# Performance work log

Measured on AMD Instinct MI355X. Metric: run time of the kernel, lower is better.

## Reference

```python
import jax, jax.numpy as jnp
import numpy as np

T, B, H, L = 1024, 256, 120, 4  # time, batch, hidden, layers


def setup_inputs() -> dict:
    key = jax.random.key(0)
    ks = jax.random.split(key, 10)
    s = 1.0 / np.sqrt(H)  # PyTorch LSTM init scale
    u = lambda k, shape: jax.random.uniform(k, shape, jnp.float32, -s, s)
    return {
        "x": jax.random.normal(ks[0], (T, B), jnp.float32),
        "h0": jax.random.uniform(ks[1], (L, B, H), jnp.float32),
        "c0": jax.random.uniform(ks[2], (L, B, H), jnp.float32),
        "W_ih0": u(ks[3], (4 * H, 1)),
        "W_ih": u(ks[4], (L - 1, 4 * H, H)),
        "W_hh": u(ks[5], (L, 4 * H, H)),
        "b_ih": u(ks[6], (L, 4 * H)),
        "b_hh": u(ks[7], (L, 4 * H)),
        "W_lin": u(ks[8], (1, H)),
        "b_lin": u(ks[9], (1,)),
    }


def _lstm_cell(x, h, c, gates_x):
    # gates_x: precomputed x @ W_ih^T + b_ih part already folded by caller
    raise NotImplementedError  # unused helper placeholder


def reference(x, h0, c0, W_ih0, W_ih, W_hh, b_ih, b_hh, W_lin, b_lin):
    def step(carry, x_t):
        h, c = carry                      # each [L, B, H]
        inp = x_t[:, None]                # [B, 1]
        new_h, new_c = [], []
        for l in range(L):
            Wih = W_ih0 if l == 0 else W_ih[l - 1]
            gates = inp @ Wih.T + b_ih[l] + h[l] @ W_hh[l].T + b_hh[l]  # [B, 4H]
            i_g, f_g, g_g, o_g = jnp.split(gates, 4, axis=-1)  # PyTorch gate order i,f,g,o
            c_l = jax.nn.sigmoid(f_g) * c[l] + jax.nn.sigmoid(i_g) * jnp.tanh(g_g)
            h_l = jax.nn.sigmoid(o_g) * jnp.tanh(c_l)
            new_h.append(h_l)
            new_c.append(c_l)
            inp = h_l
        out_t = (inp @ W_lin.T + b_lin)[:, 0]  # [B]
        return (jnp.stack(new_h), jnp.stack(new_c)), out_t

    _, outputs = jax.lax.scan(step, (h0, c0), x)  # outputs: [T, B]
    return outputs
```

## Files before the change

### kernel.cpp

```cpp
#include <hip/hip_runtime.h>
#include <hip/hip_fp16.h>
#include <math.h>

#define Tn 1024
#define Bn 256
#define Hn 120
#define Ln 4
#define NBC 16
#define NBCOL 16
#define NBLK (Ln*NBC)
#define THR 512
#define Dd 16
#define PADI 32
#define KPh 392

typedef _Float16 f16x8 __attribute__((ext_vector_type(8)));
typedef float    f32x4 __attribute__((ext_vector_type(4)));
typedef unsigned int u32x4 __attribute__((ext_vector_type(4)));
typedef unsigned short ushort_t;

template<int N> struct IC { static constexpr int value = N; };

__device__ ushort_t g_ring[(size_t)3 * Dd * NBC * NBCOL * Hn];
__device__ int g_prod[3 * NBC * PADI];
__device__ int g_cons[Ln * NBC * PADI];
__device__ int g_abort;

__global__ __launch_bounds__(256) void init_kernel() {
    int idx = threadIdx.x;
    if (idx < 3 * NBC)  g_prod[idx * PADI] = -1;
    if (idx < Ln * NBC) g_cons[idx * PADI] = -1;
    if (idx == 0)       g_abort = 0;
}

#if __has_builtin(__builtin_amdgcn_exp2f)
__device__ __forceinline__ float hw_exp2(float x) { return __builtin_amdgcn_exp2f(x); }
#else
__device__ __forceinline__ float hw_exp2(float x) { return exp2f(x); }
#endif
#if __has_builtin(__builtin_amdgcn_rcpf)
__device__ __forceinline__ float hw_rcp(float x) { return __builtin_amdgcn_rcpf(x); }
#else
__device__ __forceinline__ float hw_rcp(float x) { return 1.0f / x; }
#endif
#define LOG2E_F 1.44269504f

__device__ __forceinline__ float sigm(float v) {
    return hw_rcp(1.0f + hw_exp2(-LOG2E_F * v));
}
__device__ __forceinline__ float tanh_fast(float v) {
    return 1.0f - 2.0f * hw_rcp(1.0f + hw_exp2(2.0f * LOG2E_F * v));
}

#define BAR_LGKM() asm volatile("s_waitcnt lgkmcnt(0)\ns_barrier" ::: "memory")

__device__ __forceinline__ void spin_wait(int* p, int tgt, int& dead, int& pc) {
    if (dead || pc >= tgt) return;
    int guard = 0, v;
    while ((v = __hip_atomic_load(p, __ATOMIC_RELAXED,
                                  __HIP_MEMORY_SCOPE_SYSTEM)) < tgt) {
        __builtin_amdgcn_s_sleep(1);
        if ((++guard & 127) == 0) {
            if (__hip_atomic_load(&g_abort, __ATOMIC_RELAXED,
                                  __HIP_MEMORY_SCOPE_SYSTEM)) { dead = 1; return; }
            if (guard > 60000) { atomicExch(&g_abort, 1); dead = 1; return; }
        }
    }
    pc = v;
}

__device__ __forceinline__ void post_flag(int* p, int v) {
    __hip_atomic_store(p, v, __ATOMIC_RELAXED, __HIP_MEMORY_SCOPE_SYSTEM);
}

__global__ __launch_bounds__(THR, 2) void lstm_kernel(
    const float* __restrict__ x,    const float* __restrict__ h0,
    const float* __restrict__ c0,   const float* __restrict__ Wih0,
    const float* __restrict__ Wih,  const float* __restrict__ Whh,
    const float* __restrict__ bih,  const float* __restrict__ bhh,
    const float* __restrict__ Wlin, const float* __restrict__ blin,
    float* __restrict__ out)
{
    __shared__ _Float16 hxT[NBCOL * KPh];

    const int bx   = blockIdx.x;
    const int l    = bx >> 4;
    const int bc   = bx & 15;
    const int tid  = threadIdx.x;
    const int w    = tid >> 6;
    const int lane = tid & 63;
    const int quad = lane >> 4;
    const int l16  = lane & 15;
    const int bg0  = bc * NBCOL;
    const int mtn  = (w < 6) ? 4 : 3;
    const int mt0  = (w < 6) ? 4 * w : 24 + 3 * (w - 6);
    int dead = 0, pcb = -0x40000000, pca = -0x40000000;

    const float* WhhL = Whh + (size_t)l * 4 * Hn * Hn;
    const float* WihL = (l > 0) ? Wih + (size_t)(l - 1) * 4 * Hn * Hn : Whh;
    ushort_t* ringP = g_ring + (size_t)l * Dd * NBC * NBCOL * Hn;
    const ushort_t* ringC =
        g_ring + (size_t)(l > 0 ? l - 1 : 0) * Dd * NBC * NBCOL * Hn;
    int* prodUp = &g_prod[(l > 0 ? ((l - 1) * NBC + bc) : 0) * PADI];
    int* prodMe = &g_prod[(l < 3 ? (l * NBC + bc) : 0) * PADI];
    int* consDn = &g_cons[(l < 3 ? ((l + 1) * NBC + bc) : 0) * PADI];
    int* consMe = &g_cons[(l * NBC + bc) * PADI];

    f16x8 a[4][8];
    #pragma unroll
    for (int m = 0; m < 4; ++m) {
        int rp = (mt0 + m) * 16 + l16;
        int cell = rp >> 2, gate = rp & 3;
        int orow = gate * Hn + cell;
        #pragma unroll
        for (int kt = 0; kt < 8; ++kt) {
            f16x8 av;
            #pragma unroll
            for (int j = 0; j < 8; ++j) {
                int k = kt * 32 + quad * 8 + j;
                float v = 0.f;
                if (m < mtn) {
                    if (k < Hn)            v = WhhL[orow * Hn + k];
                    else if (l == 0)       v = (k == Hn) ? Wih0[orow] : 0.f;
                    else if (k < 2 * Hn)   v = WihL[orow * Hn + (k - Hn)];
                }
                av[j] = (_Float16)v;
            }
            a[m][kt] = av;
        }
    }

    float bias_g[4][4];
    float cst[4];
    #pragma unroll
    for (int m = 0; m < 4; ++m) {
        int cell = (mt0 + m) * 4 + quad;
        #pragma unroll
        for (int g = 0; g < 4; ++g)
            bias_g[m][g] = (m < mtn)
                ? bih[l * 4 * Hn + g * Hn + cell] + bhh[l * 4 * Hn + g * Hn + cell]
                : 0.f;
        cst[m] = (m < mtn) ? c0[(l * Bn + bg0 + l16) * Hn + cell] : 0.f;
    }

    const int cp_c = tid / 15, cp_g = tid % 15;
    const int oc_col = tid >> 3, oc_j = tid & 7;
    float wl[15];
    if (l == 3) {
        #pragma unroll
        for (int c2 = 0; c2 < 15; ++c2) wl[c2] = Wlin[oc_j * 15 + c2];
    }

    for (int q = tid; q < NBCOL * Hn; q += THR) {
        int col = q / Hn, cell = q % Hn;
        hxT[col * KPh + 256 + cell] = (_Float16)h0[(l * Bn + bg0 + col) * Hn + cell];
    }
    for (int q = tid; q < NBCOL * 136; q += THR) {
        int col = q / 136, kk = 120 + q % 136;
        hxT[col * KPh + kk] = (_Float16)0.f;
    }
    __syncthreads();

    if (l > 0) {
        spin_wait(prodUp, 0, dead, pcb);
        u32x4 v0 = {0,0,0,0};
        const ushort_t* base = ringC + ((size_t)(0 * NBC + bc)) * NBCOL * Hn;
        if (tid < 240) {
            const ushort_t* p = base + cp_c * Hn + cp_g * 8;
            asm volatile("global_load_dwordx4 %0, %1, off sc0 sc1"
                         : "=v"(v0) : "v"(p));
        }
        asm volatile("s_waitcnt vmcnt(0)" ::: "memory");
        if (tid < 240)
            *(u32x4*)&hxT[cp_c * KPh + 120 + cp_g * 8] = v0;
        __syncthreads();
        if (tid == 96) post_flag(consMe, 0);
    } else {
        if (tid < NBCOL) hxT[tid * KPh + 120] = (_Float16)x[bg0 + tid];
        __syncthreads();
    }

    auto run = [&](auto ktlc) {
        constexpr int KTL = decltype(ktlc)::value;
        for (int t = 0; t < Tn; ++t) {
            const int slotW = t & (Dd - 1);
            const int slotR = (t + 1) & (Dd - 1);
            const int hbR = ((t & 1) ^ 1) << 8;
            const int hbW = (t & 1) << 8;

            if ((t & 3) == 0) {
                if (l > 0) {
                    int tgt = (t + 4 < Tn) ? t + 4 : Tn - 1;
                    spin_wait(prodUp, tgt, dead, pcb);
                }
                if (l < 3 && t >= 16)
                    spin_wait(consDn, t - 13, dead, pca);
            }

            u32x4 ld = {0, 0, 0, 0};
            float xr = 0.f;
            if (l > 0 && (t + 1) < Tn && tid < 240) {
                const ushort_t* p = ringC + (size_t)(slotR * NBC + bc) * NBCOL * Hn
                                  + cp_c * Hn + cp_g * 8;
                asm volatile("global_load_dwordx4 %0, %1, off sc0 sc1"
                             : "=v"(ld) : "v"(p));
            }
            if (l == 0 && (t + 1) < Tn && tid < NBCOL)
                xr = x[(t + 1) * Bn + bg0 + tid];

            f32x4 acc[4];
            #pragma unroll
            for (int m = 0; m < 4; ++m) {
                f32x4 z; z[0] = bias_g[m][0]; z[1] = bias_g[m][1];
                z[2] = bias_g[m][2]; z[3] = bias_g[m][3];
                acc[m] = z;
            }

            #pragma unroll
            for (int half = 0; half < 2; ++half) {
                const int M0 = half * 2;
                #pragma unroll
                for (int kt = 0; kt < KTL; ++kt) {
                    const int e0 = kt * 32 + quad * 8;
                    const int ao = e0 + ((e0 < 120) ? hbR : 0);
                    f16x8 bfr = *(const f16x8*)&hxT[l16 * KPh + ao];
                    #pragma unroll
                    for (int m = M0; m < M0 + 2; ++m)
                        if (m < mtn)
                            acc[m] = __builtin_amdgcn_mfma_f32_16x16x32_f16(
                                a[m][kt], bfr, acc[m], 0, 0, 0);
                }
                #pragma unroll
                for (int m = M0; m < M0 + 2; ++m) {
                    if (m >= mtn) continue;
                    int cell = (mt0 + m) * 4 + quad;
                    float ig = sigm(acc[m][0]);
                    float fg = sigm(acc[m][1]);
                    float gg = tanh_fast(acc[m][2]);
                    float og = sigm(acc[m][3]);
                    float cn = fmaf(fg, cst[m], ig * gg);
                    cst[m] = cn;
                    float hn = og * tanh_fast(cn);
                    hxT[l16 * KPh + hbW + cell] = (_Float16)hn;
                }
            }
            BAR_LGKM();

            asm volatile("s_waitcnt vmcnt(0)" ::: "memory");
            __builtin_amdgcn_sched_barrier(0);

            if (l > 0 && (t + 1) < Tn && tid < 240)
                *(u32x4*)&hxT[cp_c * KPh + 120 + cp_g * 8] = ld;
            if (l == 0 && (t + 1) < Tn && tid < NBCOL)
                hxT[tid * KPh + 120] = (_Float16)xr;

            if (l < 3 && tid < 240) {
                u32x4 v0 = *(const u32x4*)&hxT[cp_c * KPh + hbW + cp_g * 8];
                ushort_t* p0 = ringP + (size_t)(slotW * NBC + bc) * NBCOL * Hn
                             + cp_c * Hn + cp_g * 8;
                asm volatile("global_store_dwordx4 %0, %1, off sc0 sc1"
                             :: "v"(p0), "v"(v0) : "memory");
            }
            if (l == 3 && tid < NBCOL * 8) {
                float pout = 0.f;
                const _Float16* hrow = &hxT[oc_col * KPh + hbW + oc_j * 15];
                #pragma unroll
                for (int c2 = 0; c2 < 15; ++c2)
                    pout = fmaf(wl[c2], (float)hrow[c2], pout);
                pout += __shfl_down(pout, 4, 8);
                pout += __shfl_down(pout, 2, 8);
                pout += __shfl_down(pout, 1, 8);
                if (oc_j == 0) out[t * Bn + bg0 + oc_col] = pout + blin[0];
            }
            BAR_LGKM();

            if ((t & 3) == 3) {
                if (l < 3 && tid == 0)  post_flag(prodMe, t - 1);
                if (l > 0 && tid == 96) post_flag(consMe, t + 1);
            }
        }
    };
    if (l == 0) run(IC<4>{});
    else        run(IC<8>{});

    if (l < 3) {
        asm volatile("s_waitcnt vmcnt(0)" ::: "memory");
        __syncthreads();
        if (tid == 0) post_flag(prodMe, Tn - 1);
    }
}

extern "C" void kernel_launch(void* const* d_in, const int* in_sizes, int n_in,
                              void* d_out, int out_size, void* d_ws, size_t ws_size,
                              hipStream_t stream) {
    const float* x    = (const float*)d_in[0];
    const float* h0   = (const float*)d_in[1];
    const float* c0   = (const float*)d_in[2];
    const float* Wih0 = (const float*)d_in[3];
    const float* Wih  = (const float*)d_in[4];
    const float* Whh  = (const float*)d_in[5];
    const float* bih  = (const float*)d_in[6];
    const float* bhh  = (const float*)d_in[7];
    const float* Wlin = (const float*)d_in[8];
    const float* blin = (const float*)d_in[9];
    float* out = (float*)d_out;

    hipLaunchKernelGGL(init_kernel, dim3(1), dim3(256), 0, stream);
    hipLaunchKernelGGL(lstm_kernel, dim3(NBLK), dim3(THR), 0, stream,
                       x, h0, c0, Wih0, Wih, Whh, bih, bhh, Wlin, blin, out);
}
```

Measured before the change: 1.697 ms.

## Store hidden state in MFMA-register order to remove one barrier per step

Each wave now writes its freshly computed h values straight from registers to the inter-layer ring in a permuted layout. The next layer reads it with dwordx2 loads, and its W_ih columns are permuted at load time to match that layout. The input part of hxT is double-buffered, which lets one of the two per-step block barriers and the LDS re-read before the global store be removed. The costs are a larger LDS row pitch, a bigger ring buffer, and tricky correctness in the buffer-parity and vmcnt ordering.

```diff
diff --git a/kernel.cpp b/kernel.cpp
--- a/kernel.cpp
+++ b/kernel.cpp
@@ -12,16 +12,17 @@
 #define THR 512
 #define Dd 16
 #define PADI 32
-#define KPh 392
+#define KPh 520
+#define ENT 2048
 
 typedef _Float16 f16x8 __attribute__((ext_vector_type(8)));
 typedef float    f32x4 __attribute__((ext_vector_type(4)));
-typedef unsigned int u32x4 __attribute__((ext_vector_type(4)));
+typedef unsigned int u32x2 __attribute__((ext_vector_type(2)));
 typedef unsigned short ushort_t;
 
 template<int N> struct IC { static constexpr int value = N; };
 
-__device__ ushort_t g_ring[(size_t)3 * Dd * NBC * NBCOL * Hn];
+__device__ ushort_t g_ring[(size_t)3 * Dd * NBC * ENT];
 __device__ int g_prod[3 * NBC * PADI];
 __device__ int g_cons[Ln * NBC * PADI];
 __device__ int g_abort;
@@ -98,9 +99,9 @@
 
     const float* WhhL = Whh + (size_t)l * 4 * Hn * Hn;
     const float* WihL = (l > 0) ? Wih + (size_t)(l - 1) * 4 * Hn * Hn : Whh;
-    ushort_t* ringP = g_ring + (size_t)l * Dd * NBC * NBCOL * Hn;
+    ushort_t* ringP = g_ring + (size_t)l * Dd * NBC * ENT;
     const ushort_t* ringC =
-        g_ring + (size_t)(l > 0 ? l - 1 : 0) * Dd * NBC * NBCOL * Hn;
+        g_ring + (size_t)(l > 0 ? l - 1 : 0) * Dd * NBC * ENT;
     int* prodUp = &g_prod[(l > 0 ? ((l - 1) * NBC + bc) : 0) * PADI];
     int* prodMe = &g_prod[(l < 3 ? (l * NBC + bc) : 0) * PADI];
     int* consDn = &g_cons[(l < 3 ? ((l + 1) * NBC + bc) : 0) * PADI];
@@ -120,9 +121,16 @@
                 int k = kt * 32 + quad * 8 + j;
                 float v = 0.f;
                 if (m < mtn) {
-                    if (k < Hn)            v = WhhL[orow * Hn + k];
-                    else if (l == 0)       v = (k == Hn) ? Wih0[orow] : 0.f;
-                    else if (k < 2 * Hn)   v = WihL[orow * Hn + (k - Hn)];
+                    if (k < Hn)          v = WhhL[orow * Hn + k];
+                    else if (l == 0)     { if (k == 120) v = Wih0[orow]; }
+                    else if (k >= 128) {
+                        int s = k - 128, w2 = s >> 4, r = s & 15;
+                        int q2 = r >> 2, m2 = r & 3;
+                        int mtn2 = (w2 < 6) ? 4 : 3;
+                        int mt02 = (w2 < 6) ? 4 * w2 : 24 + 3 * (w2 - 6);
+                        if (m2 < mtn2)
+                            v = WihL[orow * Hn + (mt02 + m2) * 4 + q2];
+                    }
                 }
                 av[j] = (_Float16)v;
             }
@@ -143,7 +151,11 @@
         cst[m] = (m < mtn) ? c0[(l * Bn + bg0 + l16) * Hn + cell] : 0.f;
     }
 
-    const int cp_c = tid / 15, cp_g = tid % 15;
+    const int sg_col = (tid >> 2) & 15;
+    const int sg_w   = tid >> 6;
+    const int sg_q   = tid & 3;
+    const int sg_lds = sg_col * KPh + 128 + sg_w * 16 + sg_q * 4;
+
     const int oc_col = tid >> 3, oc_j = tid & 7;
     float wl[15];
     if (l == 3) {
@@ -151,32 +163,26 @@
         for (int c2 = 0; c2 < 15; ++c2) wl[c2] = Wlin[oc_j * 15 + c2];
     }
 
-    for (int q = tid; q < NBCOL * Hn; q += THR) {
-        int col = q / Hn, cell = q % Hn;
+    for (int q2 = tid; q2 < NBCOL * KPh; q2 += THR) hxT[q2] = (_Float16)0.f;
+    __syncthreads();
+    for (int q2 = tid; q2 < NBCOL * Hn; q2 += THR) {
+        int col = q2 / Hn, cell = q2 % Hn;
         hxT[col * KPh + 256 + cell] = (_Float16)h0[(l * Bn + bg0 + col) * Hn + cell];
-    }
-    for (int q = tid; q < NBCOL * 136; q += THR) {
-        int col = q / 136, kk = 120 + q % 136;
-        hxT[col * KPh + kk] = (_Float16)0.f;
     }
     __syncthreads();
 
     if (l > 0) {
         spin_wait(prodUp, 0, dead, pcb);
-        u32x4 v0 = {0,0,0,0};
-        const ushort_t* base = ringC + ((size_t)(0 * NBC + bc)) * NBCOL * Hn;
-        if (tid < 240) {
-            const ushort_t* p = base + cp_c * Hn + cp_g * 8;
-            asm volatile("global_load_dwordx4 %0, %1, off sc0 sc1"
-                         : "=v"(v0) : "v"(p));
-        }
+        u32x2 v0 = {0, 0};
+        const ushort_t* p = ringC + (size_t)(0 * NBC + bc) * ENT + tid * 4;
+        asm volatile("global_load_dwordx2 %0, %1, off sc0 sc1"
+                     : "=v"(v0) : "v"(p));
         asm volatile("s_waitcnt vmcnt(0)" ::: "memory");
-        if (tid < 240)
-            *(u32x4*)&hxT[cp_c * KPh + 120 + cp_g * 8] = v0;
+        *(u32x2*)&hxT[sg_lds] = v0;
         __syncthreads();
         if (tid == 96) post_flag(consMe, 0);
     } else {
-        if (tid < NBCOL) hxT[tid * KPh + 120] = (_Float16)x[bg0 + tid];
+        if (tid < NBCOL) hxT[tid * KPh + 256 + 120] = (_Float16)x[bg0 + tid];
         __syncthreads();
     }
 
@@ -185,8 +191,9 @@
         for (int t = 0; t < Tn; ++t) {
             const int slotW = t & (Dd - 1);
             const int slotR = (t + 1) & (Dd - 1);
-            const int hbR = ((t & 1) ^ 1) << 8;
-            const int hbW = (t & 1) << 8;
+            const int q  = t & 1;
+            const int hR = (q ^ 1) << 8;
+            const int hW = q << 8;
 
             if ((t & 3) == 0) {
                 if (l > 0) {
@@ -197,12 +204,11 @@
                     spin_wait(consDn, t - 13, dead, pca);
             }
 
-            u32x4 ld = {0, 0, 0, 0};
+            u32x2 ld = {0, 0};
             float xr = 0.f;
-            if (l > 0 && (t + 1) < Tn && tid < 240) {
-                const ushort_t* p = ringC + (size_t)(slotR * NBC + bc) * NBCOL * Hn
-                                  + cp_c * Hn + cp_g * 8;
-                asm volatile("global_load_dwordx4 %0, %1, off sc0 sc1"
+            if (l > 0 && (t + 1) < Tn) {
+                const ushort_t* p = ringC + (size_t)(slotR * NBC + bc) * ENT + tid * 4;
+                asm volatile("global_load_dwordx2 %0, %1, off sc0 sc1"
                              : "=v"(ld) : "v"(p));
             }
             if (l == 0 && (t + 1) < Tn && tid < NBCOL)
@@ -215,6 +221,7 @@
                 z[2] = bias_g[m][2]; z[3] = bias_g[m][3];
                 acc[m] = z;
             }
+            unsigned short hb[4] = {0, 0, 0, 0};
 
             #pragma unroll
             for (int half = 0; half < 2; ++half) {
@@ -222,7 +229,7 @@
                 #pragma unroll
                 for (int kt = 0; kt < KTL; ++kt) {
                     const int e0 = kt * 32 + quad * 8;
-                    const int ao = e0 + ((e0 < 120) ? hbR : 0);
+                    const int ao = e0 + ((kt < 4) ? hR : (q << 8));
                     f16x8 bfr = *(const f16x8*)&hxT[l16 * KPh + ao];
                     #pragma unroll
                     for (int m = M0; m < M0 + 2; ++m)
@@ -241,29 +248,36 @@
                     float cn = fmaf(fg, cst[m], ig * gg);
                     cst[m] = cn;
                     float hn = og * tanh_fast(cn);
-                    hxT[l16 * KPh + hbW + cell] = (_Float16)hn;
+                    _Float16 hh = (_Float16)hn;
+                    hxT[l16 * KPh + hW + cell] = hh;
+                    hb[m] = __builtin_bit_cast(unsigned short, hh);
                 }
             }
+
+            if (l < 3) {
+                u32x2 sv;
+                sv[0] = (unsigned)hb[0] | ((unsigned)hb[1] << 16);
+                sv[1] = (unsigned)hb[2] | ((unsigned)hb[3] << 16);
+                ushort_t* p0 = ringP + (size_t)(slotW * NBC + bc) * ENT
+                             + w * 256 + l16 * 16 + quad * 4;
+                asm volatile("global_store_dwordx2 %0, %1, off sc0 sc1"
+                             :: "v"(p0), "v"(sv) : "memory");
+            }
+
+            if (l < 3) { asm volatile("s_waitcnt vmcnt(1)" ::: "memory"); }
+            else       { asm volatile("s_waitcnt vmcnt(0)" ::: "memory"); }
+            __builtin_amdgcn_sched_barrier(0);
+
+            if (l > 0 && (t + 1) < Tn)
+                *(u32x2*)&hxT[sg_lds + ((q ^ 1) << 8)] = ld;
+            if (l == 0 && (t + 1) < Tn && tid < NBCOL)
+                hxT[tid * KPh + hW + 120] = (_Float16)xr;
+
             BAR_LGKM();
 
-            asm volatile("s_waitcnt vmcnt(0)" ::: "memory");
-            __builtin_amdgcn_sched_barrier(0);
-
-            if (l > 0 && (t + 1) < Tn && tid < 240)
-                *(u32x4*)&hxT[cp_c * KPh + 120 + cp_g * 8] = ld;
-            if (l == 0 && (t + 1) < Tn && tid < NBCOL)
-                hxT[tid * KPh + 120] = (_Float16)xr;
-
-            if (l < 3 && tid < 240) {
-                u32x4 v0 = *(const u32x4*)&hxT[cp_c * KPh + hbW + cp_g * 8];
-                ushort_t* p0 = ringP + (size_t)(slotW * NBC + bc) * NBCOL * Hn
-                             + cp_c * Hn + cp_g * 8;
-                asm volatile("global_store_dwordx4 %0, %1, off sc0 sc1"
-                             :: "v"(p0), "v"(v0) : "memory");
-            }
             if (l == 3 && tid < NBCOL * 8) {
                 float pout = 0.f;
-                const _Float16* hrow = &hxT[oc_col * KPh + hbW + oc_j * 15];
+                const _Float16* hrow = &hxT[oc_col * KPh + hW + oc_j * 15];
                 #pragma unroll
                 for (int c2 = 0; c2 < 15; ++c2)
                     pout = fmaf(wl[c2], (float)hrow[c2], pout);
@@ -272,7 +286,6 @@
                 pout += __shfl_down(pout, 1, 8);
                 if (oc_j == 0) out[t * Bn + bg0 + oc_col] = pout + blin[0];
             }
-            BAR_LGKM();
 
             if ((t & 3) == 3) {
                 if (l < 3 && tid == 0)  post_flag(prodMe, t - 1);
```

Result: faster. 1.532 ms, median of 2 (-9.7%).
